# Performance work log

Measured on AMD Instinct MI355X. Metric: run time of the kernel, lower is better.

The kernel has to match this reference:

```python
import jax, jax.numpy as jnp
import numpy as np

# ---- static tree topology: forest of full binary trees ----
N_TREES, DEPTH = 128, 10
C, M, L, N_GEN = 16, 256, 2, 8
NODES_PER_TREE = 2 ** DEPTH - 1          # 1023
N = N_TREES * NODES_PER_TREE             # 130944 nodes


def _build_tree():
    node = np.arange(NODES_PER_TREE)
    pos1 = (node - 1) % L
    pos1[0] = 0                           # root position unused in fwd
    offs = (np.arange(N_TREES) * NODES_PER_TREE)[:, None]
    pos = np.tile(pos1, N_TREES).astype(np.int32)
    levels = []                            # top level first, as in torch code
    for k in range(1, DEPTH):
        ch1 = np.arange(2 ** k - 1, 2 ** (k + 1) - 1)
        pa1 = (ch1 - 1) // 2
        ch = (offs + ch1[None, :]).reshape(-1).astype(np.int32)
        pa = (offs + pa1[None, :]).reshape(-1).astype(np.int32)
        u1 = np.arange(2 ** (k - 1) - 1, 2 ** k - 1)   # unique parents (static)
        u = (offs + u1[None, :]).reshape(-1).astype(np.int32)
        levels.append((pa, ch, u))
    leaves1 = np.arange(2 ** (DEPTH - 1) - 1, NODES_PER_TREE)
    leaves = (offs + leaves1[None, :]).reshape(-1).astype(np.int32)
    batch = np.repeat(np.arange(N_TREES), NODES_PER_TREE).astype(np.int32)
    return pos, levels, leaves, batch

POS, LEVELS, LEAVES, BATCH = _build_tree()


def setup_inputs() -> dict:
    key = jax.random.key(0)
    k1, k2, k3, k4, k5 = jax.random.split(key, 5)
    return {
        "lambda_A": jax.random.normal(k1, (C, C, L, N_GEN), dtype=jnp.float32),
        "lambda_B": jax.random.normal(k2, (C, M, N_GEN), dtype=jnp.float32),
        "lambda_Pi": jax.random.normal(k3, (C, L, N_GEN), dtype=jnp.float32),
        "lambda_SP": jax.random.normal(k4, (L, N_GEN), dtype=jnp.float32),
        "x": jax.random.randint(k5, (N,), 0, M, dtype=jnp.int32),
    }


def reference(lambda_A, lambda_B, lambda_Pi, lambda_SP, x):
    # per-generator softmaxes (vectorized over the n_gen loop of the torch code)
    A = jax.nn.softmax(lambda_A, axis=0)    # (C,C,L,G)
    B = jax.nn.softmax(lambda_B, axis=1)    # (C,M,G)
    Pi = jax.nn.softmax(lambda_Pi, axis=0)  # (C,L,G)
    SP = jax.nn.softmax(lambda_SP, axis=0)  # (L,G)

    pos = jnp.asarray(POS)
    beta = jnp.zeros((N, C, N_GEN), dtype=lambda_A.dtype)
    t_beta = jnp.zeros_like(beta)
    ll = jnp.zeros((N, N_GEN), dtype=lambda_A.dtype)

    # leaves: beta = Pi[:,pos] * B[:,x], normalized per node
    bl = (Pi[:, pos[LEAVES]] * B[:, x[LEAVES]]).transpose(1, 0, 2)  # (nl,C,G)
    nu = bl.sum(axis=1)                                             # (nl,G)
    beta = beta.at[LEAVES].set(bl / nu[:, None])
    ll = ll.at[LEAVES].set(jnp.log(nu))

    # bottom-up recurrence over levels
    for pa, ch, u in reversed(LEVELS):
        pch = pos[ch]                                   # (E,)
        # contract children beliefs with transitions for every position, then
        # select per-edge position: avoids materializing (E,C,C,G)
        t_full = jnp.einsum('ablg,ebg->ealg', A, beta[ch])          # (E,C,L,G)
        t_ch = jnp.take_along_axis(
            t_full, pch[:, None, None, None].astype(jnp.int32), axis=2
        )[:, :, 0, :]                                               # (E,C,G)
        t_ch = t_ch * SP[pch][:, None, :]
        t_beta = t_beta.at[pa].add(t_ch)                # scatter-add to parents
        b_u = t_beta[u] * B[:, x[u]].transpose(1, 0, 2)             # (U,C,G)
        nu = b_u.sum(axis=1)
        beta = beta.at[u].set(b_u / nu[:, None])
        ll = ll.at[u].set(jnp.log(nu))

    # per-tree log likelihood: scatter(ll, batch)
    return jax.ops.segment_sum(ll, jnp.asarray(BATCH), num_segments=N_TREES)
```

## Files before the change

kernel.cpp:

```cpp
#include <hip/hip_runtime.h>

#define G_   8
#define NT_  128
#define NPT_ 1023
#define SBS  20

typedef __fp16 half8 __attribute__((ext_vector_type(8)));
typedef __fp16 half4v __attribute__((ext_vector_type(4)));
typedef float f32x4 __attribute__((ext_vector_type(4)));
#define RCP(x) __builtin_amdgcn_rcpf(x)

template<int R>
__device__ __forceinline__ float rotr16(float v) {
  return __int_as_float(__builtin_amdgcn_update_dpp(
      0, __float_as_int(v), 0x120 | R, 0xF, 0xF, true));
}
__device__ __forceinline__ float grpsum16(float v) {
  v += rotr16<8>(v); v += rotr16<4>(v); v += rotr16<2>(v); v += rotr16<1>(v);
  return v;
}
__device__ __forceinline__ float grpmax16(float v) {
  v = fmaxf(v, rotr16<8>(v)); v = fmaxf(v, rotr16<4>(v));
  v = fmaxf(v, rotr16<2>(v)); v = fmaxf(v, rotr16<1>(v));
  return v;
}

__device__ __forceinline__ float colsum(float s) {
  float t = s;
  asm("s_nop 1\n\t"
      "v_permlane16_swap_b32 %0, %1" : "+v"(s), "+v"(t));
  s = s + t;
  float u = s;
  asm("s_nop 1\n\t"
      "v_permlane32_swap_b32 %0, %1" : "+v"(s), "+v"(u));
  return s + u;
}

__device__ __forceinline__ half4v leafstep(const float* __restrict__ sB, int m0,
                                           int xv, float p0, float p1,
                                           float p2, float p3, float& nuOut) {
  f32x4 b = *(const f32x4*)(sB + xv + m0);
  float r0 = b[0] * p0, r1 = b[1] * p1, r2 = b[2] * p2, r3 = b[3] * p3;
  float nu = colsum((r0 + r1) + (r2 + r3));
  nuOut = nu;
  float rc = RCP(nu);
  half4v p;
  p[0] = (__fp16)(r0 * rc); p[1] = (__fp16)(r1 * rc);
  p[2] = (__fp16)(r2 * rc); p[3] = (__fp16)(r3 * rc);
  return p;
}

__device__ __forceinline__ half4v istep(const float* __restrict__ sB, int m0,
                                        int xv, half8 af, half4v pl, half4v pr,
                                        float nuL, float nuR,
                                        float& nuOut, float& ll) {
  half8 bb;
  bb[0] = pl[0]; bb[1] = pl[1]; bb[2] = pl[2]; bb[3] = pl[3];
  bb[4] = pr[0]; bb[5] = pr[1]; bb[6] = pr[2]; bb[7] = pr[3];
  f32x4 z = {0.f, 0.f, 0.f, 0.f};
  f32x4 acc = __builtin_amdgcn_mfma_f32_16x16x32_f16(af, bb, z, 0, 0, 0);
  ll += __log2f(nuL * nuR);
  f32x4 b = *(const f32x4*)(sB + xv + m0);
  float r0 = acc[0] * b[0], r1 = acc[1] * b[1];
  float r2 = acc[2] * b[2], r3 = acc[3] * b[3];
  float nu = colsum((r0 + r1) + (r2 + r3));
  nuOut = nu;
  float rc = RCP(nu);
  half4v p;
  p[0] = (__fp16)(r0 * rc); p[1] = (__fp16)(r1 * rc);
  p[2] = (__fp16)(r2 * rc); p[3] = (__fp16)(r3 * rc);
  return p;
}

__device__ __forceinline__ void topstep(const float* __restrict__ rb, int rs,
                                        float* wb, int ws, int U, int xv,
                                        const float* __restrict__ sB, int m0,
                                        int col, half8 af, float& ll) {
  bool valid = col < U;
  int tc = valid ? col : 0;
  half8 bb;
  #pragma unroll
  for (int i = 0; i < 4; ++i) {
    bb[i]     = (__fp16)rb[(m0 + i) * rs + 2 * tc];
    bb[4 + i] = (__fp16)rb[(m0 + i) * rs + 2 * tc + 1];
  }
  f32x4 z = {0.f, 0.f, 0.f, 0.f};
  f32x4 acc = __builtin_amdgcn_mfma_f32_16x16x32_f16(af, bb, z, 0, 0, 0);
  f32x4 b = *(const f32x4*)(sB + xv + m0);
  float r0 = acc[0] * b[0], r1 = acc[1] * b[1];
  float r2 = acc[2] * b[2], r3 = acc[3] * b[3];
  float nu = colsum((r0 + r1) + (r2 + r3));
  float rc = RCP(nu);
  if (valid) {
    ll += __log2f(nu);
    if (wb) {
      wb[(m0 + 0) * ws + col] = r0 * rc;
      wb[(m0 + 1) * ws + col] = r1 * rc;
      wb[(m0 + 2) * ws + col] = r2 * rc;
      wb[(m0 + 3) * ws + col] = r3 * rc;
    }
  }
  __syncthreads();
}

__global__ __launch_bounds__(256, 4) void htmm_fwd_kernel(
    const float* __restrict__ lA,
    const float* __restrict__ lB,
    const float* __restrict__ lPi,
    const float* __restrict__ lSP,
    const int*   __restrict__ x,
    float*       __restrict__ out)
{
  __shared__ float sB[256 * SBS];
  __shared__ float sA[2 * 16 * 16];
  __shared__ float sPi[32];
  __shared__ float rootsA[16 * 65];
  __shared__ float rootsB[16 * 33];
  __shared__ float red[4];

  const int tid = threadIdx.x;
  const int bid = blockIdx.x;
  const int T   = bid >> 3;
  const int g   = bid & 7;
  const int lane = tid & 63;
  const int wv   = tid >> 6;
  const int c    = lane & 15;
  const int col  = (wv << 4) | c;
  const int m0   = (lane >> 4) << 2;
  const int a    = tid & 15;
  const int grp  = tid >> 4;
  const long base = (long)T * NPT_;

  int xl[8], x8[4], x7[2], xt[6];
  #pragma unroll
  for (int j = 0; j < 8; ++j) xl[j] = x[base + 511 + 8 * col + j] * SBS;
  #pragma unroll
  for (int t = 0; t < 4; ++t) x8[t] = x[base + 255 + 4 * col + t] * SBS;
  #pragma unroll
  for (int t = 0; t < 2; ++t) x7[t] = x[base + 127 + 2 * col + t] * SBS;
  const int x6 = x[base + 63 + col] * SBS;
  #pragma unroll
  for (int lvl = 0; lvl < 6; ++lvl) {
    int U = 1 << lvl;
    int tc = (col < U) ? col : (U - 1);
    xt[lvl] = x[base + (U - 1) + tc] * SBS;
  }

  float s0 = lSP[g], s1 = lSP[G_ + g];
  float sm = fmaxf(s0, s1);
  float e0 = __expf(s0 - sm), e1 = __expf(s1 - sm);
  float inv = RCP(e0 + e1);
  const float SP0 = e0 * inv, SP1 = e1 * inv;

  #pragma unroll
  for (int l = 0; l < 2; ++l) {
    float v = lA[a * 256 + grp * 16 + l * 8 + g];
    float m = grpmax16(v);
    float e = __expf(v - m);
    float s = grpsum16(e);
    sA[(l * 16 + grp) * 16 + a] = e * RCP(s);
  }
  if (grp < 2) {
    float v = lPi[a * 16 + grp * 8 + g];
    float m = grpmax16(v);
    float e = __expf(v - m);
    float s = grpsum16(e);
    sPi[grp * 16 + a] = e * RCP(s);
  }
  {
    const int cc = grp;
    float vv[16];
    float mx = -1e30f;
    #pragma unroll
    for (int k = 0; k < 16; ++k) {
      vv[k] = lB[cc * (256 * G_) + (a + 16 * k) * G_ + g];
      mx = fmaxf(mx, vv[k]);
    }
    mx = grpmax16(mx);
    float ssum = 0.f;
    #pragma unroll
    for (int k = 0; k < 16; ++k) { vv[k] = __expf(vv[k] - mx); ssum += vv[k]; }
    ssum = grpsum16(ssum);
    float is = RCP(ssum);
    #pragma unroll
    for (int k = 0; k < 16; ++k) sB[(a + 16 * k) * SBS + cc] = vv[k] * is;
  }
  __syncthreads();

  half8 af;
  #pragma unroll
  for (int i = 0; i < 4; ++i) {
    af[i]     = (__fp16)(sA[(m0 + i) * 16 + c] * SP0);
    af[4 + i] = (__fp16)(sA[(16 + m0 + i) * 16 + c] * SP1);
  }
  const float pi00 = sPi[m0 + 0], pi01 = sPi[m0 + 1];
  const float pi02 = sPi[m0 + 2], pi03 = sPi[m0 + 3];
  const float pi10 = sPi[16 + m0 + 0], pi11 = sPi[16 + m0 + 1];
  const float pi12 = sPi[16 + m0 + 2], pi13 = sPi[16 + m0 + 3];

  float ll = 0.f;

  half4v t0, t1, p80, p81, q0, q1;
  float nl0, nl1, n80, n81, n70, n71;
  t0 = leafstep(sB, m0, xl[0], pi00, pi01, pi02, pi03, nl0);
  t1 = leafstep(sB, m0, xl[1], pi10, pi11, pi12, pi13, nl1);
  p80 = istep(sB, m0, x8[0], af, t0, t1, nl0, nl1, n80, ll);
  t0 = leafstep(sB, m0, xl[2], pi00, pi01, pi02, pi03, nl0);
  t1 = leafstep(sB, m0, xl[3], pi10, pi11, pi12, pi13, nl1);
  p81 = istep(sB, m0, x8[1], af, t0, t1, nl0, nl1, n81, ll);
  q0 = istep(sB, m0, x7[0], af, p80, p81, n80, n81, n70, ll);
  t0 = leafstep(sB, m0, xl[4], pi00, pi01, pi02, pi03, nl0);
  t1 = leafstep(sB, m0, xl[5], pi10, pi11, pi12, pi13, nl1);
  p80 = istep(sB, m0, x8[2], af, t0, t1, nl0, nl1, n80, ll);
  t0 = leafstep(sB, m0, xl[6], pi00, pi01, pi02, pi03, nl0);
  t1 = leafstep(sB, m0, xl[7], pi10, pi11, pi12, pi13, nl1);
  p81 = istep(sB, m0, x8[3], af, t0, t1, nl0, nl1, n81, ll);
  q1 = istep(sB, m0, x7[1], af, p80, p81, n80, n81, n71, ll);

  {
    half8 bb;
    bb[0] = q0[0]; bb[1] = q0[1]; bb[2] = q0[2]; bb[3] = q0[3];
    bb[4] = q1[0]; bb[5] = q1[1]; bb[6] = q1[2]; bb[7] = q1[3];
    f32x4 z = {0.f, 0.f, 0.f, 0.f};
    f32x4 acc = __builtin_amdgcn_mfma_f32_16x16x32_f16(af, bb, z, 0, 0, 0);
    f32x4 b = *(const f32x4*)(sB + x6 + m0);
    float r0 = acc[0] * b[0], r1 = acc[1] * b[1];
    float r2 = acc[2] * b[2], r3 = acc[3] * b[3];
    float nu = colsum((r0 + r1) + (r2 + r3));
    ll += __log2f(n70 * n71 * nu);
    float rc = RCP(nu);
    rootsA[(m0 + 0) * 65 + col] = r0 * rc;
    rootsA[(m0 + 1) * 65 + col] = r1 * rc;
    rootsA[(m0 + 2) * 65 + col] = r2 * rc;
    rootsA[(m0 + 3) * 65 + col] = r3 * rc;
  }
  __syncthreads();

  topstep(rootsA, 65, rootsB, 33, 32, xt[5], sB, m0, col, af, ll);
  topstep(rootsB, 33, rootsA, 65, 16, xt[4], sB, m0, col, af, ll);
  topstep(rootsA, 65, rootsB, 33,  8, xt[3], sB, m0, col, af, ll);
  topstep(rootsB, 33, rootsA, 65,  4, xt[2], sB, m0, col, af, ll);
  topstep(rootsA, 65, rootsB, 33,  2, xt[1], sB, m0, col, af, ll);
  topstep(rootsB, 33, nullptr, 0,  1, xt[0], sB, m0, col, af, ll);

  float v = ll;
  #pragma unroll
  for (int off = 32; off > 0; off >>= 1) v += __shfl_down(v, off, 64);
  if (lane == 0) red[wv] = v;
  __syncthreads();
  if (tid == 0)
    out[bid] = (red[0] + red[1] + red[2] + red[3]) *
               (0.6931471805599453f * 0.25f);
}

extern "C" void kernel_launch(void* const* d_in, const int* in_sizes, int n_in,
                              void* d_out, int out_size, void* d_ws, size_t ws_size,
                              hipStream_t stream) {
  const float* lA  = (const float*)d_in[0];
  const float* lB  = (const float*)d_in[1];
  const float* lPi = (const float*)d_in[2];
  const float* lSP = (const float*)d_in[3];
  const int*   x   = (const int*)d_in[4];
  float* out = (float*)d_out;
  htmm_fwd_kernel<<<dim3(NT_ * G_), dim3(256), 0, stream>>>(lA, lB, lPi, lSP, x, out);
}
```

Baseline: 18.67 us.

## Keep upper tree levels in-wave via shuffles and stage x in shared memory

Result: no change. 18.46 us (-1.2%).

```diff
diff --git a/kernel.cpp b/kernel.cpp
--- a/kernel.cpp
+++ b/kernel.cpp
@@ -34,6 +34,13 @@
   asm("s_nop 1\n\t"
       "v_permlane32_swap_b32 %0, %1" : "+v"(s), "+v"(u));
   return s + u;
+}
+
+__device__ __forceinline__ half4v shfl4h(half4v v, int src) {
+  int2 iv = __builtin_bit_cast(int2, v);
+  iv.x = __shfl(iv.x, src, 16);
+  iv.y = __shfl(iv.y, src, 16);
+  return __builtin_bit_cast(half4v, iv);
 }
 
 __device__ __forceinline__ half4v leafstep(const float* __restrict__ sB, int m0,
@@ -72,6 +79,32 @@
   return p;
 }
 
+template<int UW>
+__device__ __forceinline__ half4v wstep(const float* __restrict__ sB,
+                                        const int* __restrict__ xs,
+                                        int nodebase, int m0, int c,
+                                        half8 af, half4v q, float& ll) {
+  int tc = (UW == 8) ? (c & 7) : ((c < UW) ? c : (UW - 1));
+  int xv = xs[nodebase + tc] * SBS;
+  half4v uL = shfl4h(q, 2 * tc);
+  half4v uR = shfl4h(q, 2 * tc + 1);
+  half8 bb;
+  bb[0] = uL[0]; bb[1] = uL[1]; bb[2] = uL[2]; bb[3] = uL[3];
+  bb[4] = uR[0]; bb[5] = uR[1]; bb[6] = uR[2]; bb[7] = uR[3];
+  f32x4 z = {0.f, 0.f, 0.f, 0.f};
+  f32x4 acc = __builtin_amdgcn_mfma_f32_16x16x32_f16(af, bb, z, 0, 0, 0);
+  f32x4 b = *(const f32x4*)(sB + xv + m0);
+  float r0 = acc[0] * b[0], r1 = acc[1] * b[1];
+  float r2 = acc[2] * b[2], r3 = acc[3] * b[3];
+  float nu = colsum((r0 + r1) + (r2 + r3));
+  float rc = RCP(nu);
+  if (c < UW) ll += __log2f(nu);
+  half4v p;
+  p[0] = (__fp16)(r0 * rc); p[1] = (__fp16)(r1 * rc);
+  p[2] = (__fp16)(r2 * rc); p[3] = (__fp16)(r3 * rc);
+  return p;
+}
+
 __device__ __forceinline__ void topstep(const float* __restrict__ rb, int rs,
                                         float* wb, int ws, int U, int xv,
                                         const float* __restrict__ sB, int m0,
@@ -114,8 +147,9 @@
   __shared__ float sB[256 * SBS];
   __shared__ float sA[2 * 16 * 16];
   __shared__ float sPi[32];
-  __shared__ float rootsA[16 * 65];
-  __shared__ float rootsB[16 * 33];
+  __shared__ int   xls[1024];
+  __shared__ float topL2[16 * 5];
+  __shared__ float topL1[16 * 3];
   __shared__ float red[4];
 
   const int tid = threadIdx.x;
@@ -131,19 +165,10 @@
   const int grp  = tid >> 4;
   const long base = (long)T * NPT_;
 
-  int xl[8], x8[4], x7[2], xt[6];
-  #pragma unroll
-  for (int j = 0; j < 8; ++j) xl[j] = x[base + 511 + 8 * col + j] * SBS;
-  #pragma unroll
-  for (int t = 0; t < 4; ++t) x8[t] = x[base + 255 + 4 * col + t] * SBS;
-  #pragma unroll
-  for (int t = 0; t < 2; ++t) x7[t] = x[base + 127 + 2 * col + t] * SBS;
-  const int x6 = x[base + 63 + col] * SBS;
-  #pragma unroll
-  for (int lvl = 0; lvl < 6; ++lvl) {
-    int U = 1 << lvl;
-    int tc = (col < U) ? col : (U - 1);
-    xt[lvl] = x[base + (U - 1) + tc] * SBS;
+  #pragma unroll
+  for (int j = 0; j < 4; ++j) {
+    int idx = tid + 256 * j;
+    if (idx < NPT_) xls[idx + 1] = x[base + idx];
   }
 
   float s0 = lSP[g], s1 = lSP[G_ + g];
@@ -187,6 +212,8 @@
   }
   __syncthreads();
 
+  const int* xs = xls + 1;
+
   half8 af;
   #pragma unroll
   for (int i = 0; i < 4; ++i) {
@@ -198,50 +225,82 @@
   const float pi10 = sPi[16 + m0 + 0], pi11 = sPi[16 + m0 + 1];
   const float pi12 = sPi[16 + m0 + 2], pi13 = sPi[16 + m0 + 3];
 
+  int xl[8], x8v[4], x7v[2];
+  #pragma unroll
+  for (int j = 0; j < 8; ++j) xl[j] = xs[511 + 8 * col + j] * SBS;
+  #pragma unroll
+  for (int t = 0; t < 4; ++t) x8v[t] = xs[255 + 4 * col + t] * SBS;
+  #pragma unroll
+  for (int t = 0; t < 2; ++t) x7v[t] = xs[127 + 2 * col + t] * SBS;
+  const int x6v = xs[63 + col] * SBS;
+
   float ll = 0.f;
 
   half4v t0, t1, p80, p81, q0, q1;
   float nl0, nl1, n80, n81, n70, n71;
   t0 = leafstep(sB, m0, xl[0], pi00, pi01, pi02, pi03, nl0);
   t1 = leafstep(sB, m0, xl[1], pi10, pi11, pi12, pi13, nl1);
-  p80 = istep(sB, m0, x8[0], af, t0, t1, nl0, nl1, n80, ll);
+  p80 = istep(sB, m0, x8v[0], af, t0, t1, nl0, nl1, n80, ll);
   t0 = leafstep(sB, m0, xl[2], pi00, pi01, pi02, pi03, nl0);
   t1 = leafstep(sB, m0, xl[3], pi10, pi11, pi12, pi13, nl1);
-  p81 = istep(sB, m0, x8[1], af, t0, t1, nl0, nl1, n81, ll);
-  q0 = istep(sB, m0, x7[0], af, p80, p81, n80, n81, n70, ll);
+  p81 = istep(sB, m0, x8v[1], af, t0, t1, nl0, nl1, n81, ll);
+  q0 = istep(sB, m0, x7v[0], af, p80, p81, n80, n81, n70, ll);
   t0 = leafstep(sB, m0, xl[4], pi00, pi01, pi02, pi03, nl0);
   t1 = leafstep(sB, m0, xl[5], pi10, pi11, pi12, pi13, nl1);
-  p80 = istep(sB, m0, x8[2], af, t0, t1, nl0, nl1, n80, ll);
+  p80 = istep(sB, m0, x8v[2], af, t0, t1, nl0, nl1, n80, ll);
   t0 = leafstep(sB, m0, xl[6], pi00, pi01, pi02, pi03, nl0);
   t1 = leafstep(sB, m0, xl[7], pi10, pi11, pi12, pi13, nl1);
-  p81 = istep(sB, m0, x8[3], af, t0, t1, nl0, nl1, n81, ll);
-  q1 = istep(sB, m0, x7[1], af, p80, p81, n80, n81, n71, ll);
-
+  p81 = istep(sB, m0, x8v[3], af, t0, t1, nl0, nl1, n81, ll);
+  q1 = istep(sB, m0, x7v[1], af, p80, p81, n80, n81, n71, ll);
+
+  half4v q6;
   {
     half8 bb;
     bb[0] = q0[0]; bb[1] = q0[1]; bb[2] = q0[2]; bb[3] = q0[3];
     bb[4] = q1[0]; bb[5] = q1[1]; bb[6] = q1[2]; bb[7] = q1[3];
     f32x4 z = {0.f, 0.f, 0.f, 0.f};
     f32x4 acc = __builtin_amdgcn_mfma_f32_16x16x32_f16(af, bb, z, 0, 0, 0);
-    f32x4 b = *(const f32x4*)(sB + x6 + m0);
+    f32x4 b = *(const f32x4*)(sB + x6v + m0);
     float r0 = acc[0] * b[0], r1 = acc[1] * b[1];
     float r2 = acc[2] * b[2], r3 = acc[3] * b[3];
     float nu = colsum((r0 + r1) + (r2 + r3));
     ll += __log2f(n70 * n71 * nu);
     float rc = RCP(nu);
-    rootsA[(m0 + 0) * 65 + col] = r0 * rc;
-    rootsA[(m0 + 1) * 65 + col] = r1 * rc;
-    rootsA[(m0 + 2) * 65 + col] = r2 * rc;
-    rootsA[(m0 + 3) * 65 + col] = r3 * rc;
+    q6[0] = (__fp16)(r0 * rc); q6[1] = (__fp16)(r1 * rc);
+    q6[2] = (__fp16)(r2 * rc); q6[3] = (__fp16)(r3 * rc);
+  }
+
+  half4v q5 = wstep<8>(sB, xs, 31 + 8 * wv, m0, c, af, q6, ll);
+  half4v q4 = wstep<4>(sB, xs, 15 + 4 * wv, m0, c, af, q5, ll);
+  half4v q3 = wstep<2>(sB, xs,  7 + 2 * wv, m0, c, af, q4, ll);
+  {
+    int xv = xs[3 + wv] * SBS;
+    half4v uL = shfl4h(q3, 0);
+    half4v uR = shfl4h(q3, 1);
+    half8 bb;
+    bb[0] = uL[0]; bb[1] = uL[1]; bb[2] = uL[2]; bb[3] = uL[3];
+    bb[4] = uR[0]; bb[5] = uR[1]; bb[6] = uR[2]; bb[7] = uR[3];
+    f32x4 z = {0.f, 0.f, 0.f, 0.f};
+    f32x4 acc = __builtin_amdgcn_mfma_f32_16x16x32_f16(af, bb, z, 0, 0, 0);
+    f32x4 b = *(const f32x4*)(sB + xv + m0);
+    float r0 = acc[0] * b[0], r1 = acc[1] * b[1];
+    float r2 = acc[2] * b[2], r3 = acc[3] * b[3];
+    float nu = colsum((r0 + r1) + (r2 + r3));
+    float rc = RCP(nu);
+    if (c == 0) {
+      ll += __log2f(nu);
+      topL2[(m0 + 0) * 5 + wv] = r0 * rc;
+      topL2[(m0 + 1) * 5 + wv] = r1 * rc;
+      topL2[(m0 + 2) * 5 + wv] = r2 * rc;
+      topL2[(m0 + 3) * 5 + wv] = r3 * rc;
+    }
   }
   __syncthreads();
 
-  topstep(rootsA, 65, rootsB, 33, 32, xt[5], sB, m0, col, af, ll);
-  topstep(rootsB, 33, rootsA, 65, 16, xt[4], sB, m0, col, af, ll);
-  topstep(rootsA, 65, rootsB, 33,  8, xt[3], sB, m0, col, af, ll);
-  topstep(rootsB, 33, rootsA, 65,  4, xt[2], sB, m0, col, af, ll);
-  topstep(rootsA, 65, rootsB, 33,  2, xt[1], sB, m0, col, af, ll);
-  topstep(rootsB, 33, nullptr, 0,  1, xt[0], sB, m0, col, af, ll);
+  int xvL1 = xs[1 + ((col < 2) ? col : 0)] * SBS;
+  topstep(topL2, 5, topL1, 3, 2, xvL1, sB, m0, col, af, ll);
+  int xvL0 = xs[0] * SBS;
+  topstep(topL1, 3, nullptr, 0, 1, xvL0, sB, m0, col, af, ll);
 
   float v = ll;
   #pragma unroll
```
